# Kernel optimization log

Hardware: AMD Instinct MI355X
Metric: run time of the kernel (lower is better)

Reference implementation:

```python
import jax, jax.numpy as jnp
import numpy as np

EPS = 1e-12  # F.normalize default eps


def _l2_normalize(x):
    n = jnp.linalg.norm(x, axis=-1, keepdims=True)
    return x / jnp.maximum(n, EPS)


def setup_inputs() -> dict:
    key = jax.random.key(0)
    k1, k2 = jax.random.split(key)
    B, N, D = 2048, 100000, 256
    query = jax.random.normal(k1, (B, D), dtype=jnp.float32)
    memory_states = jax.random.normal(k2, (N, D), dtype=jnp.float32)
    return {"query": query, "memory_states": memory_states, "k": 8}


def reference(query, memory_states, k):
    # cosine-similarity retrieval: normalize both sides, dense matmul, top-k, gather
    mem_norm = _l2_normalize(memory_states)          # [N, D]
    query_norm = _l2_normalize(query)                # [B, D]
    scores = query_norm @ mem_norm.T                 # [B, N]
    top_k_scores, indices = jax.lax.top_k(scores, k)  # [B, k] each
    retrieved = memory_states[indices]               # [B, k, D] (raw, un-normalized states as in torch)
    return retrieved, top_k_scores
```

## Files before the change

kernel.cpp:

```cpp
#include <hip/hip_runtime.h>
#include <hip/hip_bf16.h>
#include <stdint.h>

#define DIM 256
#define TOPK 8
#define NSTRIPS 64
#define STRIP_TOP 8
#define QT 256
#define NT 32
#define CAND (NSTRIPS * STRIP_TOP)
#define RESCORE 64
#define IDXMASK 0x1FFFFu

typedef __attribute__((ext_vector_type(8))) short short8;
typedef __attribute__((ext_vector_type(4))) float floatx4;
typedef __attribute__((address_space(3))) unsigned int lds_u32;
typedef __attribute__((address_space(1))) const unsigned int gbl_u32;

__device__ __forceinline__ unsigned short f2bf(float f) {
    union { float f; uint32_t u; } v; v.f = f;
    uint32_t u = v.u;
    uint32_t r = u + 0x7fffu + ((u >> 16) & 1u);
    return (unsigned short)(r >> 16);
}

__device__ __forceinline__ uint32_t umaxu(uint32_t a, uint32_t b) { return a > b ? a : b; }
__device__ __forceinline__ uint32_t uminu(uint32_t a, uint32_t b) { return a < b ? a : b; }

__device__ __forceinline__ void top8_insert(uint32_t* ts, uint32_t key) {
#pragma unroll
    for (int j = 0; j < STRIP_TOP - 1; j++) {
        uint32_t m;
        asm("v_med3_u32 %0, %1, %2, %3" : "=v"(m) : "v"(ts[j]), "v"(ts[j + 1]), "v"(key));
        ts[j] = m;
    }
    ts[STRIP_TOP - 1] = umaxu(ts[STRIP_TOP - 1], key);
}

__global__ void prep_kernel(const float* __restrict__ query,
                            const float* __restrict__ mem,
                            float* __restrict__ rnorm_mem,
                            unsigned short* __restrict__ q_bf16,
                            unsigned short* __restrict__ mem_bf16,
                            int B, int N)
{
    int wave = threadIdx.x >> 6;
    int lane = threadIdx.x & 63;
    int row  = blockIdx.x * 4 + wave;
    int total = N + B;
    if (row >= total) return;
    const float* src = (row < N) ? (mem + (size_t)row * DIM)
                                 : (query + (size_t)(row - N) * DIM);
    float4 v = ((const float4*)src)[lane];
    float ss = v.x * v.x + v.y * v.y + v.z * v.z + v.w * v.w;
#pragma unroll
    for (int m = 32; m >= 1; m >>= 1) ss += __shfl_xor(ss, m, 64);
    float rinv = 1.0f / fmaxf(sqrtf(ss), 1e-12f);
    ushort4 o;
    o.x = f2bf(v.x * rinv); o.y = f2bf(v.y * rinv);
    o.z = f2bf(v.z * rinv); o.w = f2bf(v.w * rinv);
    if (row < N) {
        if (lane == 0) rnorm_mem[row] = rinv;
        if (mem_bf16) ((ushort4*)(mem_bf16 + (size_t)row * DIM))[lane] = o;
    } else {
        ((ushort4*)(q_bf16 + (size_t)(row - N) * DIM))[lane] = o;
    }
}

template<bool PRE>
__global__ __launch_bounds__(512, 4) void score_select_kernel(
    const float* __restrict__ mem,
    const float* __restrict__ rnorm_mem,
    const unsigned short* __restrict__ mem_bf16,
    const unsigned short* __restrict__ q_bf16,
    uint32_t* __restrict__ cand_key,
    int B, int N)
{
    __shared__ unsigned short lds_m[2][NT * DIM];

    const int t    = threadIdx.x;
    const int wave = t >> 6;
    const int lane = t & 63;
    const int quad = lane >> 4;
    const int l16  = lane & 15;

    const int lin  = (int)(blockIdx.x + gridDim.x * blockIdx.y);
    const int SPX  = NSTRIPS / 8;
    const int strip = (lin & 7) * SPX + ((lin >> 3) % SPX);
    const int qb    = (lin >> 3) / SPX;
    const int qbase = qb * QT;

    const int SS    = (N + NSTRIPS - 1) / NSTRIPS;
    const int n0    = strip * SS;
    const int nend  = (n0 + SS < N) ? (n0 + SS) : N;
    const int limit = nend - n0;
    const int ntiles = (limit + NT - 1) / NT;

    short8 qfrag[2][8];
#pragma unroll
    for (int b = 0; b < 2; b++) {
        int qrow = qbase + wave * 32 + b * 16 + l16;
        const unsigned short* qp = q_bf16 + (size_t)qrow * DIM + quad * 8;
#pragma unroll
        for (int ks = 0; ks < 8; ks++)
            qfrag[b][ks] = *(const short8*)(qp + ks * 32);
    }

    uint32_t ts[2][STRIP_TOP];
#pragma unroll
    for (int b = 0; b < 2; b++)
#pragma unroll
        for (int j = 0; j < STRIP_TOP; j++) ts[b][j] = 0;

    const int l5  = lane >> 5;
    const int s32 = lane & 31;

    auto stage = [&](unsigned short* lbase, int tileIdx) {
        int base = n0 + tileIdx * NT;
        if (PRE) {
#pragma unroll
            for (int is = 0; is < 2; is++) {
                int rl = is * 16 + wave * 2 + l5;
                int n = base + rl; if (n >= nend) n = nend - 1;
                int chunk = s32 ^ (rl & 7);
                const unsigned short* gp = mem_bf16 + (size_t)n * DIM + chunk * 8;
                unsigned short* lp = lbase + (is * 16 + wave * 2) * DIM;
                __builtin_amdgcn_global_load_lds((gbl_u32*)(const void*)gp,
                                                 (lds_u32*)(void*)lp, 16, 0, 0);
            }
        } else {
#pragma unroll
            for (int i = 0; i < 4; i++) {
                int rl = i * 8 + wave;
                int n = base + rl;
                ushort4 o;
                if (n < nend) {
                    float rinv = rnorm_mem[n];
                    float4 v = ((const float4*)(mem + (size_t)n * DIM))[lane];
                    o.x = f2bf(v.x * rinv); o.y = f2bf(v.y * rinv);
                    o.z = f2bf(v.z * rinv); o.w = f2bf(v.w * rinv);
                } else { o.x = 0; o.y = 0; o.z = 0; o.w = 0; }
                int slot = (lane >> 1) ^ (rl & 7);
                *(ushort4*)(lbase + rl * DIM + slot * 8 + (lane & 1) * 4) = o;
            }
        }
    };

    stage(&lds_m[0][0], 0);
    __syncthreads();

    const floatx4 bias4 = {1.125f, 1.125f, 1.125f, 1.125f};
    for (int tile = 0; tile < ntiles; tile++) {
        unsigned short* lbuf = &lds_m[tile & 1][0];
        if (tile + 1 < ntiles) stage(&lds_m[(tile + 1) & 1][0], tile + 1);

        floatx4 acc[2][2];
#pragma unroll
        for (int a = 0; a < 2; a++)
#pragma unroll
            for (int b = 0; b < 2; b++) acc[a][b] = bias4;

#pragma unroll
        for (int ks = 0; ks < 8; ks++) {
#pragma unroll
            for (int a = 0; a < 2; a++) {
                int row = a * 16 + l16;
                int slot = (ks * 4 + quad) ^ (l16 & 7);
                short8 m = *(const short8*)(lbuf + row * DIM + slot * 8);
#pragma unroll
                for (int b = 0; b < 2; b++)
                    acc[a][b] = __builtin_amdgcn_mfma_f32_16x16x32_bf16(m, qfrag[b][ks], acc[a][b], 0, 0, 0);
            }
        }

        const int tb0 = tile * NT + quad * 4;
        const bool full = (tile * NT + NT <= limit);
#pragma unroll
        for (int b = 0; b < 2; b++) {
#pragma unroll
            for (int a = 0; a < 2; a++) {
#pragma unroll
                for (int rp = 0; rp < 2; rp++) {
                    int loc0 = tb0 + a * 16 + 2 * rp;
                    uint32_t k0 = (__float_as_uint(acc[a][b][2 * rp])     & 0xFFFF0000u) | (uint32_t)loc0;
                    uint32_t k1 = (__float_as_uint(acc[a][b][2 * rp + 1]) & 0xFFFF0000u) | (uint32_t)(loc0 + 1);
                    if (!full) {
                        if (loc0 >= limit)     k0 = 0;
                        if (loc0 + 1 >= limit) k1 = 0;
                    }
                    uint32_t kmax = umaxu(k0, k1);
                    uint32_t kmin = uminu(k0, k1);
                    top8_insert(ts[b], kmax);
                    if (__any(kmin > ts[b][0]))
                        top8_insert(ts[b], kmin);
                }
            }
        }

        __syncthreads();
    }

#pragma unroll
    for (int b = 0; b < 2; b++) {
#pragma unroll
        for (int step = 32; step >= 16; step >>= 1) {
            uint32_t other[STRIP_TOP];
#pragma unroll
            for (int j = 0; j < STRIP_TOP; j++)
                other[j] = __shfl_xor(ts[b][j], step, 64);
#pragma unroll
            for (int j = 0; j < STRIP_TOP; j++)
                top8_insert(ts[b], other[j]);
        }
    }

    if (quad == 0) {
#pragma unroll
        for (int b = 0; b < 2; b++) {
            int q = qbase + wave * 32 + b * 16 + l16;
            size_t off = ((size_t)q * NSTRIPS + strip) * STRIP_TOP;
            uint4 o0, o1;
            uint32_t k;
            k = ts[b][0]; o0.x = ((k >> 17) << 17) | (uint32_t)(n0 + (int)(k & 0xFFFFu));
            k = ts[b][1]; o0.y = ((k >> 17) << 17) | (uint32_t)(n0 + (int)(k & 0xFFFFu));
            k = ts[b][2]; o0.z = ((k >> 17) << 17) | (uint32_t)(n0 + (int)(k & 0xFFFFu));
            k = ts[b][3]; o0.w = ((k >> 17) << 17) | (uint32_t)(n0 + (int)(k & 0xFFFFu));
            k = ts[b][4]; o1.x = ((k >> 17) << 17) | (uint32_t)(n0 + (int)(k & 0xFFFFu));
            k = ts[b][5]; o1.y = ((k >> 17) << 17) | (uint32_t)(n0 + (int)(k & 0xFFFFu));
            k = ts[b][6]; o1.z = ((k >> 17) << 17) | (uint32_t)(n0 + (int)(k & 0xFFFFu));
            k = ts[b][7]; o1.w = ((k >> 17) << 17) | (uint32_t)(n0 + (int)(k & 0xFFFFu));
            ((uint4*)(cand_key + off))[0] = o0;
            ((uint4*)(cand_key + off))[1] = o1;
        }
    }
}

__global__ __launch_bounds__(256) void rescore_kernel(
    const float* __restrict__ query,
    const float* __restrict__ mem,
    const uint32_t* __restrict__ cand_key,
    float* __restrict__ out,
    int B, int N)
{
    __shared__ uint32_t cs[CAND];
    __shared__ float  lds_q[DIM];
    __shared__ double red[4];
    __shared__ double qss_sh;
    __shared__ int    sel_i[RESCORE];
    __shared__ double rs[RESCORE];
    __shared__ double best_s[TOPK];
    __shared__ int    best_i[TOPK];

    const int t    = threadIdx.x;
    const int q    = blockIdx.x;
    const int lane = t & 63;
    const int wave = t >> 6;

    for (int i = t; i < CAND; i += 256)
        cs[i] = cand_key[(size_t)q * CAND + i];

    float qv = query[(size_t)q * DIM + t];
    lds_q[t] = qv;
    double p = (double)qv * (double)qv;
#pragma unroll
    for (int m = 32; m >= 1; m >>= 1) p += __shfl_xor(p, m, 64);
    if (lane == 0) red[wave] = p;
    __syncthreads();
    if (t == 0) qss_sh = red[0] + red[1] + red[2] + red[3];

    {
        uint32_t* qcs = cs + wave * 128;
        for (int k = 2; k <= 128; k <<= 1) {
            for (int j = k >> 1; j > 0; j >>= 1) {
                int i  = 2 * lane - (lane & (j - 1));
                int ip = i + j;
                bool up = ((i & k) == 0);
                uint32_t a = qcs[i], b2 = qcs[ip];
                bool aFirst = a > b2;
                bool doSwap = up ? (!aFirst) : aFirst;
                if (doSwap) { qcs[i] = b2; qcs[ip] = a; }
            }
        }
        if (lane < 16) sel_i[wave * 16 + lane] = (int)(qcs[lane] & IDXMASK);
    }
    __syncthreads();

    double qss = qss_sh;
    for (int r = 0; r < 16; r++) {
        int c = wave * 16 + r;
        int idx = sel_i[c];
        float4 mv = ((const float4*)(mem + (size_t)idx * DIM))[lane];
        float4 qv4 = ((const float4*)lds_q)[lane];
        double dqm = (double)mv.x * (double)qv4.x + (double)mv.y * (double)qv4.y
                   + (double)mv.z * (double)qv4.z + (double)mv.w * (double)qv4.w;
        double dmm = (double)mv.x * (double)mv.x + (double)mv.y * (double)mv.y
                   + (double)mv.z * (double)mv.z + (double)mv.w * (double)mv.w;
#pragma unroll
        for (int m = 32; m >= 1; m >>= 1) {
            dqm += __shfl_xor(dqm, m, 64);
            dmm += __shfl_xor(dmm, m, 64);
        }
        if (lane == 0)
            rs[c] = dqm / (fmax(sqrt(qss), 1e-12) * fmax(sqrt(dmm), 1e-12));
    }
    __syncthreads();

    if (t == 0) {
        double bs[TOPK]; int bi[TOPK];
        for (int i = 0; i < TOPK; i++) { bs[i] = -1e300; bi[i] = 0x7fffffff; }
        for (int c = 0; c < RESCORE; c++) {
            double s = rs[c]; int id = sel_i[c];
            bool better = (s > bs[TOPK - 1]) || (s == bs[TOPK - 1] && id < bi[TOPK - 1]);
            if (better) {
                int pos = TOPK - 1;
                while (pos > 0) {
                    bool b2 = (s > bs[pos - 1]) || (s == bs[pos - 1] && id < bi[pos - 1]);
                    if (!b2) break;
                    bs[pos] = bs[pos - 1]; bi[pos] = bi[pos - 1]; pos--;
                }
                bs[pos] = s; bi[pos] = id;
            }
        }
        for (int i = 0; i < TOPK; i++) { best_s[i] = bs[i]; best_i[i] = bi[i]; }
    }
    __syncthreads();

    size_t score_base = (size_t)B * TOPK * DIM;
    if (t < TOPK) out[score_base + (size_t)q * TOPK + t] = (float)best_s[t];

#pragma unroll
    for (int rep = 0; rep < 2; rep++) {
        int j  = t >> 5;
        int d4 = (t & 31) + rep * 32;
        int idx = best_i[j];
        float4 v = ((const float4*)(mem + (size_t)idx * DIM))[d4];
        ((float4*)(out + ((size_t)q * TOPK + j) * DIM))[d4] = v;
    }
}

extern "C" void kernel_launch(void* const* d_in, const int* in_sizes, int n_in,
                              void* d_out, int out_size, void* d_ws, size_t ws_size,
                              hipStream_t stream)
{
    const float* query = (const float*)d_in[0];
    const float* mem   = (const float*)d_in[1];
    int B = in_sizes[0] / DIM;
    int N = in_sizes[1] / DIM;

    auto align256 = [](size_t x) { return (x + 255) & ~(size_t)255; };
    size_t off = 0;
    auto alloc = [&](size_t bytes) { void* p = (char*)d_ws + off; off += align256(bytes); return p; };

    float* rnorm_mem       = (float*)alloc((size_t)N * 4);
    unsigned short* q_bf16 = (unsigned short*)alloc((size_t)B * DIM * 2);
    uint32_t* cand_key     = (uint32_t*)alloc((size_t)B * CAND * 4);
    size_t base_need = off;
    unsigned short* mem_bf16 = (unsigned short*)((char*)d_ws + base_need);
    bool pre = (base_need + align256((size_t)N * DIM * 2)) <= ws_size;
    if (!pre) mem_bf16 = nullptr;

    int prep_blocks = (N + B + 3) / 4;
    prep_kernel<<<prep_blocks, 256, 0, stream>>>(query, mem, rnorm_mem, q_bf16,
                                                 mem_bf16, B, N);

    dim3 g2((B + QT - 1) / QT, NSTRIPS);
    if (pre)
        score_select_kernel<true><<<g2, 512, 0, stream>>>(mem, rnorm_mem, mem_bf16, q_bf16,
                                                          cand_key, B, N);
    else
        score_select_kernel<false><<<g2, 512, 0, stream>>>(mem, rnorm_mem, mem_bf16, q_bf16,
                                                           cand_key, B, N);

    rescore_kernel<<<B, 256, 0, stream>>>(query, mem, cand_key, (float*)d_out, B, N);
}
```

Baseline: 349.6 us.

## Quad-buffer LDS tiles, compute two tiles per barrier, precompute swizzled LDS offsets

The score/select kernel now keeps four LDS tile buffers instead of two. Each loop iteration stages tiles two ahead and computes two tiles between barriers, which halves the number of __syncthreads per strip and deepens the prefetch. The swizzled LDS read addresses are also precomputed once per thread as two byte offsets, replacing the per-iteration index math. The cost is a doubling of LDS per block to 64 KB, which can cut how many blocks fit on a CU below the launch-bounds target of 4.

```diff
diff --git a/kernel.cpp b/kernel.cpp
--- a/kernel.cpp
+++ b/kernel.cpp
@@ -76,7 +76,7 @@
     uint32_t* __restrict__ cand_key,
     int B, int N)
 {
-    __shared__ unsigned short lds_m[2][NT * DIM];
+    __shared__ unsigned short lds_m[4][NT * DIM];
 
     const int t    = threadIdx.x;
     const int wave = t >> 6;
@@ -114,6 +114,9 @@
 
     const int l5  = lane >> 5;
     const int s32 = lane & 31;
+
+    const int o0 = l16 * 512 + (quad ^ (l16 & 3)) * 16 + ((l16 >> 2) & 1) * 64;
+    const int o1 = o0 ^ 64;
 
     auto stage = [&](unsigned short* lbase, int tileIdx) {
         int base = n0 + tileIdx * NT;
@@ -146,27 +149,23 @@
         }
     };
 
-    stage(&lds_m[0][0], 0);
-    __syncthreads();
-
     const floatx4 bias4 = {1.125f, 1.125f, 1.125f, 1.125f};
-    for (int tile = 0; tile < ntiles; tile++) {
-        unsigned short* lbuf = &lds_m[tile & 1][0];
-        if (tile + 1 < ntiles) stage(&lds_m[(tile + 1) & 1][0], tile + 1);
-
+
+    auto compute_tile = [&](const unsigned short* lbuf, int tile) {
         floatx4 acc[2][2];
 #pragma unroll
         for (int a = 0; a < 2; a++)
 #pragma unroll
             for (int b = 0; b < 2; b++) acc[a][b] = bias4;
 
+        const char* pb0 = (const char*)lbuf + o0;
+        const char* pb1 = (const char*)lbuf + o1;
 #pragma unroll
         for (int ks = 0; ks < 8; ks++) {
 #pragma unroll
             for (int a = 0; a < 2; a++) {
-                int row = a * 16 + l16;
-                int slot = (ks * 4 + quad) ^ (l16 & 7);
-                short8 m = *(const short8*)(lbuf + row * DIM + slot * 8);
+                const char* p = (ks & 1) ? pb1 : pb0;
+                short8 m = *(const short8*)(p + a * 8192 + (ks >> 1) * 128);
 #pragma unroll
                 for (int b = 0; b < 2; b++)
                     acc[a][b] = __builtin_amdgcn_mfma_f32_16x16x32_bf16(m, qfrag[b][ks], acc[a][b], 0, 0, 0);
@@ -196,7 +195,17 @@
                 }
             }
         }
-
+    };
+
+    stage(&lds_m[0][0], 0);
+    if (1 < ntiles) stage(&lds_m[1][0], 1);
+    __syncthreads();
+
+    for (int tp = 0; tp < ntiles; tp += 2) {
+        if (tp + 2 < ntiles) stage(&lds_m[(tp + 2) & 3][0], tp + 2);
+        if (tp + 3 < ntiles) stage(&lds_m[(tp + 3) & 3][0], tp + 3);
+        compute_tile(&lds_m[tp & 3][0], tp);
+        if (tp + 1 < ntiles) compute_tile(&lds_m[(tp + 1) & 3][0], tp + 1);
         __syncthreads();
     }
 
@@ -219,18 +228,18 @@
         for (int b = 0; b < 2; b++) {
             int q = qbase + wave * 32 + b * 16 + l16;
             size_t off = ((size_t)q * NSTRIPS + strip) * STRIP_TOP;
-            uint4 o0, o1;
+            uint4 o0v, o1v;
             uint32_t k;
-            k = ts[b][0]; o0.x = ((k >> 17) << 17) | (uint32_t)(n0 + (int)(k & 0xFFFFu));
-            k = ts[b][1]; o0.y = ((k >> 17) << 17) | (uint32_t)(n0 + (int)(k & 0xFFFFu));
-            k = ts[b][2]; o0.z = ((k >> 17) << 17) | (uint32_t)(n0 + (int)(k & 0xFFFFu));
-            k = ts[b][3]; o0.w = ((k >> 17) << 17) | (uint32_t)(n0 + (int)(k & 0xFFFFu));
-            k = ts[b][4]; o1.x = ((k >> 17) << 17) | (uint32_t)(n0 + (int)(k & 0xFFFFu));
-            k = ts[b][5]; o1.y = ((k >> 17) << 17) | (uint32_t)(n0 + (int)(k & 0xFFFFu));
-            k = ts[b][6]; o1.z = ((k >> 17) << 17) | (uint32_t)(n0 + (int)(k & 0xFFFFu));
-            k = ts[b][7]; o1.w = ((k >> 17) << 17) | (uint32_t)(n0 + (int)(k & 0xFFFFu));
-            ((uint4*)(cand_key + off))[0] = o0;
-            ((uint4*)(cand_key + off))[1] = o1;
+            k = ts[b][0]; o0v.x = ((k >> 17) << 17) | (uint32_t)(n0 + (int)(k & 0xFFFFu));
+            k = ts[b][1]; o0v.y = ((k >> 17) << 17) | (uint32_t)(n0 + (int)(k & 0xFFFFu));
+            k = ts[b][2]; o0v.z = ((k >> 17) << 17) | (uint32_t)(n0 + (int)(k & 0xFFFFu));
+            k = ts[b][3]; o0v.w = ((k >> 17) << 17) | (uint32_t)(n0 + (int)(k & 0xFFFFu));
+            k = ts[b][4]; o1v.x = ((k >> 17) << 17) | (uint32_t)(n0 + (int)(k & 0xFFFFu));
+            k = ts[b][5]; o1v.y = ((k >> 17) << 17) | (uint32_t)(n0 + (int)(k & 0xFFFFu));
+            k = ts[b][6]; o1v.z = ((k >> 17) << 17) | (uint32_t)(n0 + (int)(k & 0xFFFFu));
+            k = ts[b][7]; o1v.w = ((k >> 17) << 17) | (uint32_t)(n0 + (int)(k & 0xFFFFu));
+            ((uint4*)(cand_key + off))[0] = o0v;
+            ((uint4*)(cand_key + off))[1] = o1v;
         }
     }
 }
```

Result: no change. 345.6 us (-1.2%).
